# Kernel tuning notes

Measured on AMD Instinct MI355X. Metric: run time of the kernel, lower is better.

The kernel has to match this reference:

```python
import jax, jax.numpy as jnp
import numpy as np

NUM_TOKENS = 32000
DIM = 1024
DEPTH = 4
HEADS = 16
DIM_HEAD = 64
FF_MULT = 4
DH_FF = int(DIM * FF_MULT * 2 / 3)  # 2730
B, N = 2, 2048
ROPE_THETA = 10000.0


def setup_inputs() -> dict:
    key = jax.random.key(0)
    ks = jax.random.split(key, 8)
    s = 0.02
    return {
        "tokens": jax.random.randint(ks[0], (B, N), 0, NUM_TOKENS),
        "token_emb": jax.random.normal(ks[1], (NUM_TOKENS, DIM)) * s,
        "attn_norm_w": jnp.ones((DEPTH, DIM)),
        "wqkv": jax.random.normal(ks[2], (DEPTH, DIM, 3 * HEADS * DIM_HEAD)) * s,
        "wo": jax.random.normal(ks[3], (DEPTH, HEADS * DIM_HEAD, DIM)) * s,
        "ff_norm_w": jnp.ones((DEPTH, DIM)),
        "ff_w1": jax.random.normal(ks[4], (DEPTH, DIM, 2 * DH_FF)) * s,
        "ff_b1": jnp.zeros((DEPTH, 2 * DH_FF)),
        "ff_w2": jax.random.normal(ks[5], (DEPTH, DH_FF, DIM)) * s,
        "ff_b2": jnp.zeros((DEPTH, DIM)),
        "final_norm_w": jnp.ones((DIM,)),
        "logits_w": jax.random.normal(ks[6], (DIM, NUM_TOKENS)) * s,
        "logits_b": jnp.zeros((NUM_TOKENS,)),
    }


def rmsnorm(x, w):
    eps = jnp.finfo(x.dtype).eps  # torch RMSNorm default eps
    var = jnp.mean(jnp.square(x), axis=-1, keepdims=True)
    return x * jax.lax.rsqrt(var + eps) * w


def rotate_half(x):
    x1, x2 = jnp.split(x, 2, axis=-1)
    return jnp.concatenate((-x2, x1), axis=-1)


def apply_rope(pos, t):
    return t * jnp.cos(pos) + rotate_half(t) * jnp.sin(pos)


def reference(tokens, token_emb, attn_norm_w, wqkv, wo, ff_norm_w,
              ff_w1, ff_b1, ff_w2, ff_b2, final_norm_w, logits_w, logits_b):
    b, n = tokens.shape
    x = token_emb[tokens]  # [b, n, dim]

    # rotary embedding table [n, dim_head]
    inv_freq = ROPE_THETA ** (-(jnp.arange(0, DIM_HEAD, 2, dtype=jnp.float32) / DIM_HEAD))
    freqs = jnp.arange(n, dtype=jnp.float32)[:, None] * inv_freq[None, :]
    pos = jnp.concatenate((freqs, freqs), axis=-1)

    scale = DIM_HEAD ** -0.5
    causal = jnp.triu(jnp.ones((n, n), dtype=bool), 1)

    for l in range(DEPTH):
        # --- attention ---
        h = rmsnorm(x, attn_norm_w[l])
        qkv = jnp.einsum('bnd,de->bne', h, wqkv[l])
        qkv = qkv.reshape(b, n, 3, HEADS, DIM_HEAD)
        qkv = jnp.transpose(qkv, (2, 0, 3, 1, 4))  # [3, b, h, n, d]
        q, k, v = qkv[0], qkv[1], qkv[2]
        q = apply_rope(pos, q)
        k = apply_rope(pos, k)
        q = q * scale
        sim = jnp.einsum('bhid,bhjd->bhij', q, k)
        sim = jnp.where(causal, -jnp.finfo(sim.dtype).max, sim)
        attn = jax.nn.softmax(sim, axis=-1)
        out = jnp.einsum('bhij,bhjd->bhid', attn, v)
        out = jnp.transpose(out, (0, 2, 1, 3)).reshape(b, n, HEADS * DIM_HEAD)
        x = jnp.einsum('bne,ed->bnd', out, wo[l]) + x

        # --- GEGLU feedforward ---
        h = rmsnorm(x, ff_norm_w[l])
        u = jnp.einsum('bnd,de->bne', h, ff_w1[l]) + ff_b1[l]
        u1, gate = jnp.split(u, 2, axis=-1)
        g = jax.nn.gelu(gate, approximate=False) * u1
        x = jnp.einsum('bne,ed->bnd', g, ff_w2[l]) + ff_b2[l] + x

    embed = rmsnorm(x, final_norm_w)
    logits = jnp.einsum('bnd,dv->bnv', embed, logits_w) + logits_b
    return logits
```

## Files before the change

kernel.cpp:

```cpp
#include <hip/hip_runtime.h>
#include <math.h>
#include <stdint.h>


using short8v = __attribute__((ext_vector_type(8))) short;
using f32x4   = __attribute__((ext_vector_type(4))) float;

__device__ __forceinline__ float b2f(short s) {
    union { unsigned u; float f; } v; v.u = ((unsigned)(unsigned short)s) << 16; return v.f;
}
__device__ __forceinline__ short f2b(float f) {
    union { float f; unsigned u; } v; v.f = f;
    unsigned r = v.u + 0x7FFFu + ((v.u >> 16) & 1u);
    return (short)(r >> 16);
}

__device__ __forceinline__ void mfma_n(f32x4& d, short8v a, short8v b) {
    asm("v_mfma_f32_16x16x32_bf16 %0, %1, %2, %0" : "+v"(d) : "v"(a), "v"(b));
}
__device__ __forceinline__ void mfma_f(f32x4& d, short8v a, short8v b) {
    asm("s_nop 1\n\tv_mfma_f32_16x16x32_bf16 %0, %1, %2, %0" : "+v"(d) : "v"(a), "v"(b));
}
#define MFMA_FENCE() do { __builtin_amdgcn_sched_barrier(0); \
    asm volatile("s_nop 7\n\ts_nop 7"); \
    __builtin_amdgcn_sched_barrier(0); } while (0)

__device__ __forceinline__ void gload16(const void* g, void* l) {
    __builtin_amdgcn_global_load_lds(
        (const __attribute__((address_space(1))) unsigned int*)(uintptr_t)g,
        (__attribute__((address_space(3))) unsigned int*)(uintptr_t)l,
        16, 0, 0);
}

__global__ void rope_table_k(float* __restrict__ ct, float* __restrict__ st) {
    int i = blockIdx.x * 256 + threadIdx.x;
    int n = i >> 5, j = i & 31;
    float freq = expf(-(float)j * (9.210340371976184f / 32.f));
    float a = (float)n * freq;
    ct[i] = cosf(a);
    st[i] = sinf(a);
}

__global__ void embed_k(const int* __restrict__ tok, const float* __restrict__ emb,
                        float* __restrict__ x) {
    int row = blockIdx.x;
    int tk = tok[row];
    const float4* src = (const float4*)(emb + (size_t)tk * 1024);
    float4* dst = (float4*)(x + (size_t)row * 1024);
    dst[threadIdx.x] = src[threadIdx.x];
}

__global__ void wconv_k(const float* __restrict__ W, short* __restrict__ T,
                        int K, int N, int Kpad,
                        size_t w_lstride, size_t t_lstride) {
    W += blockIdx.z * w_lstride;
    T += blockIdx.z * t_lstride;
    int n0 = blockIdx.x * 32, k0 = blockIdx.y * 32;
    __shared__ float tile[32][33];
    int t = threadIdx.x;
    int kk = t >> 3, ns = (t & 7) * 4;
    float4 v = make_float4(0.f, 0.f, 0.f, 0.f);
    int gk = k0 + kk;
    if (gk < K) {
        if (n0 + ns + 3 < N) {
            v = *(const float4*)(W + (size_t)gk * N + n0 + ns);
        } else {
            float tmp[4] = {0.f, 0.f, 0.f, 0.f};
            #pragma unroll
            for (int j = 0; j < 4; ++j)
                if (n0 + ns + j < N) tmp[j] = W[(size_t)gk * N + n0 + ns + j];
            v = make_float4(tmp[0], tmp[1], tmp[2], tmp[3]);
        }
    }
    tile[kk][ns + 0] = v.x; tile[kk][ns + 1] = v.y;
    tile[kk][ns + 2] = v.z; tile[kk][ns + 3] = v.w;
    __syncthreads();
    int nn = t >> 3, ks = (t & 7) * 4;
    short o[4];
    #pragma unroll
    for (int j = 0; j < 4; ++j) o[j] = f2b(tile[ks + j][nn]);
    *(int2*)(T + (size_t)(n0 + nn) * Kpad + k0 + ks) = *(int2*)o;
}

__global__ void rmsnorm_k(const float* __restrict__ x, const float* __restrict__ wt,
                          short* __restrict__ out) {
    int row = blockIdx.x;
    int t = threadIdx.x;
    const float* xr = x + (size_t)row * 1024;
    float4 v = ((const float4*)xr)[t];
    float ss = v.x * v.x + v.y * v.y + v.z * v.z + v.w * v.w;
    #pragma unroll
    for (int off = 32; off > 0; off >>= 1) ss += __shfl_down(ss, off, 64);
    __shared__ float red[4];
    if ((t & 63) == 0) red[t >> 6] = ss;
    __syncthreads();
    float tot = red[0] + red[1] + red[2] + red[3];
    float inv = rsqrtf(tot * (1.f / 1024.f) + 1.1920929e-7f);
    float4 wv = ((const float4*)wt)[t];
    int2 pk;
    pk.x = (int)(unsigned short)f2b(v.x * inv * wv.x) |
           ((int)(unsigned short)f2b(v.y * inv * wv.y) << 16);
    pk.y = (int)(unsigned short)f2b(v.z * inv * wv.z) |
           ((int)(unsigned short)f2b(v.w * inv * wv.w) << 16);
    *(int2*)(out + (size_t)row * 1024 + t * 4) = pk;
}

__global__ void rope_apply_k(short* __restrict__ qkv, const float* __restrict__ ct,
                             const float* __restrict__ st) {
    int gidx = blockIdx.x * 256 + threadIdx.x;
    int j  = gidx & 31;
    int r  = (gidx >> 5) & 4095;
    int hk = gidx >> 17;
    int qk = hk >> 4, h = hk & 15;
    int n = r & 2047;
    size_t base = (size_t)r * 3072 + (size_t)qk * 1024 + h * 64 + j;
    float a  = b2f(qkv[base]);
    float bv = b2f(qkv[base + 32]);
    float cc = ct[n * 32 + j], sv = st[n * 32 + j];
    float na = a * cc - bv * sv;
    float nb = bv * cc + a * sv;
    if (qk == 0) { na *= 0.125f; nb *= 0.125f; }
    qkv[base]      = f2b(na);
    qkv[base + 32] = f2b(nb);
}

__global__ void vt_k(const short* __restrict__ qkv, short* __restrict__ vt) {
    int id = blockIdx.x * 256 + threadIdx.x;
    int dt = id & 7, nt = (id >> 3) & 255, bh = id >> 11;
    int b = bh >> 4, h = bh & 15;
    short s[8][8];
    #pragma unroll
    for (int r = 0; r < 8; ++r)
        *(int4*)s[r] = *(const int4*)(qkv + (size_t)(b * 2048 + nt * 8 + r) * 3072
                                      + 2048 + h * 64 + dt * 8);
    #pragma unroll
    for (int cc = 0; cc < 8; ++cc) {
        short o4[8];
        #pragma unroll
        for (int r = 0; r < 8; ++r) o4[r] = s[r][cc];
        *(int4*)(vt + (size_t)(bh * 64 + dt * 8 + cc) * 2048 + nt * 8) = *(int4*)o4;
    }
}

__global__ void geglu_k(const short* __restrict__ u, short* __restrict__ gbuf) {
    int r = blockIdx.x;
    int c = blockIdx.y * 256 + threadIdx.x;
    if (c >= 2752) return;
    float v = 0.f;
    if (c < 2730) {
        float u1 = b2f(u[(size_t)r * 5460 + c]);
        float gt = b2f(u[(size_t)r * 5460 + 2730 + c]);
        v = 0.5f * gt * (1.f + erff(gt * 0.7071067811865475f)) * u1;
    }
    gbuf[(size_t)r * 2752 + c] = f2b(v);
}

template <bool BIAS, bool RES, bool OUTBF16>
__global__ __launch_bounds__(256, 2) void gemm2(
    const short* __restrict__ A, const short* __restrict__ Bt,
    const float* __restrict__ bias, const float* __restrict__ res,
    void* __restrict__ outp, int N, int lda, int ldb, int ksteps) {
    __shared__ __align__(16) short As[128 * 32];
    __shared__ __align__(16) short Bs[128 * 32];
    const int t = threadIdx.x;
    const int lane = t & 63;
    const int w = t >> 6, wm = w >> 1, wn = w & 1;
    const int c = lane & 15, g = lane >> 4;

    const int nwg = (int)gridDim.x;
    const int cpx = nwg >> 3;
    const int wg = ((int)blockIdx.x & 7) * cpx + ((int)blockIdx.x >> 3);
    const int m0 = (wg & 31) << 7;
    const int n0 = (wg >> 5) << 7;

    const int srow = w * 32 + (lane >> 2);
    const int sseg = (lane & 3) * 8;
    const short* ga0 = A  + (size_t)(m0 + srow) * lda + sseg;
    const short* ga1 = A  + (size_t)(m0 + srow + 16) * lda + sseg;
    const short* gb0 = Bt + (size_t)(n0 + srow) * ldb + sseg;
    const short* gb1 = Bt + (size_t)(n0 + srow + 16) * ldb + sseg;
    short* la0 = &As[(w * 2 + 0) * 512];
    short* la1 = &As[(w * 2 + 1) * 512];
    short* lb0 = &Bs[(w * 2 + 0) * 512];
    short* lb1 = &Bs[(w * 2 + 1) * 512];

    f32x4 acc[4][4] = {};

    for (int kt = 0; kt < ksteps; ++kt) {
        const int k0 = kt << 5;
        __syncthreads();
        gload16(ga0 + k0, la0);
        gload16(ga1 + k0, la1);
        gload16(gb0 + k0, lb0);
        gload16(gb1 + k0, lb1);
        __syncthreads();
        short8v af[4], bf[4];
        #pragma unroll
        for (int mi = 0; mi < 4; ++mi)
            af[mi] = *(const short8v*)&As[(wm * 64 + mi * 16 + c) * 32 + g * 8];
        #pragma unroll
        for (int ni = 0; ni < 4; ++ni)
            bf[ni] = *(const short8v*)&Bs[(wn * 64 + ni * 16 + c) * 32 + g * 8];
        #pragma unroll
        for (int mi = 0; mi < 4; ++mi)
            #pragma unroll
            for (int ni = 0; ni < 4; ++ni)
                mfma_n(acc[mi][ni], af[mi], bf[ni]);
    }
    MFMA_FENCE();
    #pragma unroll
    for (int mi = 0; mi < 4; ++mi) {
        #pragma unroll
        for (int ni = 0; ni < 4; ++ni) {
            int col = n0 + wn * 64 + ni * 16 + c;
            if (col < N) {
                float bv = BIAS ? bias[col] : 0.f;
                #pragma unroll
                for (int i = 0; i < 4; ++i) {
                    int row = m0 + wm * 64 + mi * 16 + g * 4 + i;
                    size_t off = (size_t)row * N + col;
                    float v = acc[mi][ni][i] + bv;
                    if (RES) v += res[off];
                    if (OUTBF16) ((short*)outp)[off] = f2b(v);
                    else         ((float*)outp)[off] = v;
                }
            }
        }
    }
}

__global__ __launch_bounds__(256, 2) void attn_fwd(
    const short* __restrict__ qkv, const short* __restrict__ vt,
    short* __restrict__ o) {
    const int qt = blockIdx.x, bh = blockIdx.y;
    const int b = bh >> 4, h = bh & 15;
    const int t = threadIdx.x, lane = t & 63, w = t >> 6;
    const int c = lane & 15, g = lane >> 4;
    __shared__ __align__(16) short Ks[128 * 72];
    __shared__ __align__(16) short Vs[64 * 136];
    __shared__ __align__(16) short Ps[128 * 136];

    #pragma unroll
    for (int i = 0; i < 4; ++i) {
        int idx = t + i * 256, r = idx >> 3, seg = idx & 7;
        *(int4*)&Ps[r * 136 + seg * 8] =
            *(const int4*)(qkv + (size_t)(b * 2048 + qt * 128 + r) * 3072 + h * 64 + seg * 8);
    }
    __syncthreads();
    short8v qf[2][2];
    #pragma unroll
    for (int mi = 0; mi < 2; ++mi)
        #pragma unroll
        for (int kk = 0; kk < 2; ++kk)
            qf[mi][kk] = *(const short8v*)&Ps[(w * 32 + mi * 16 + c) * 136 + kk * 32 + g * 8];

    f32x4 oacc[2][4] = {};
    float mrow[2][4], lrow[2][4];
    #pragma unroll
    for (int mi = 0; mi < 2; ++mi)
        #pragma unroll
        for (int i = 0; i < 4; ++i) { mrow[mi][i] = -3.0e38f; lrow[mi][i] = 0.f; }

    for (int jt = 0; jt <= qt; ++jt) {
        __syncthreads();
        #pragma unroll
        for (int i = 0; i < 4; ++i) {
            int idx = t + i * 256, r = idx >> 3, seg = idx & 7;
            *(int4*)&Ks[r * 72 + seg * 8] =
                *(const int4*)(qkv + (size_t)(b * 2048 + jt * 128 + r) * 3072
                               + 1024 + h * 64 + seg * 8);
        }
        #pragma unroll
        for (int i = 0; i < 4; ++i) {
            int idx = t + i * 256, d = idx >> 4, seg = idx & 15;
            *(int4*)&Vs[d * 136 + seg * 8] =
                *(const int4*)(vt + (size_t)(bh * 64 + d) * 2048 + jt * 128 + seg * 8);
        }
        __syncthreads();
        f32x4 sacc[2][8] = {};
        #pragma unroll
        for (int kk = 0; kk < 2; ++kk) {
            short8v kf[8];
            #pragma unroll
            for (int ni = 0; ni < 8; ++ni)
                kf[ni] = *(const short8v*)&Ks[(ni * 16 + c) * 72 + kk * 32 + g * 8];
            #pragma unroll
            for (int mi = 0; mi < 2; ++mi)
                #pragma unroll
                for (int ni = 0; ni < 8; ++ni) {
                    if (kk == 0) mfma_f(sacc[mi][ni], qf[mi][kk], kf[ni]);
                    else         mfma_n(sacc[mi][ni], qf[mi][kk], kf[ni]);
                }
        }
        MFMA_FENCE();
        if (jt == qt) {
            #pragma unroll
            for (int mi = 0; mi < 2; ++mi)
                #pragma unroll
                for (int ni = 0; ni < 8; ++ni)
                    #pragma unroll
                    for (int i = 0; i < 4; ++i) {
                        int qrow = w * 32 + mi * 16 + g * 4 + i;
                        int kcol = ni * 16 + c;
                        if (kcol > qrow) sacc[mi][ni][i] = -3.0e38f;
                    }
        }
        #pragma unroll
        for (int mi = 0; mi < 2; ++mi) {
            #pragma unroll
            for (int i = 0; i < 4; ++i) {
                float mx = sacc[mi][0][i];
                #pragma unroll
                for (int ni = 1; ni < 8; ++ni) mx = fmaxf(mx, sacc[mi][ni][i]);
                #pragma unroll
                for (int off = 1; off < 16; off <<= 1) mx = fmaxf(mx, __shfl_xor(mx, off, 64));
                float mnew = fmaxf(mrow[mi][i], mx);
                float alpha = __expf(mrow[mi][i] - mnew);
                mrow[mi][i] = mnew;
                float ls = 0.f;
                #pragma unroll
                for (int ni = 0; ni < 8; ++ni) {
                    float p = __expf(sacc[mi][ni][i] - mnew);
                    sacc[mi][ni][i] = p;
                    ls += p;
                }
                #pragma unroll
                for (int off = 1; off < 16; off <<= 1) ls += __shfl_xor(ls, off, 64);
                lrow[mi][i] = lrow[mi][i] * alpha + ls;
                #pragma unroll
                for (int df = 0; df < 4; ++df) oacc[mi][df][i] *= alpha;
            }
        }
        #pragma unroll
        for (int mi = 0; mi < 2; ++mi)
            #pragma unroll
            for (int ni = 0; ni < 8; ++ni)
                #pragma unroll
                for (int i = 0; i < 4; ++i)
                    Ps[(w * 32 + mi * 16 + g * 4 + i) * 136 + ni * 16 + c] =
                        f2b(sacc[mi][ni][i]);
        #pragma unroll
        for (int kk = 0; kk < 4; ++kk) {
            short8v pf[2], vf[4];
            #pragma unroll
            for (int mi = 0; mi < 2; ++mi)
                pf[mi] = *(const short8v*)&Ps[(w * 32 + mi * 16 + c) * 136 + kk * 32 + g * 8];
            #pragma unroll
            for (int df = 0; df < 4; ++df)
                vf[df] = *(const short8v*)&Vs[(df * 16 + c) * 136 + kk * 32 + g * 8];
            #pragma unroll
            for (int mi = 0; mi < 2; ++mi)
                #pragma unroll
                for (int df = 0; df < 4; ++df) {
                    if (kk == 0) mfma_f(oacc[mi][df], pf[mi], vf[df]);
                    else         mfma_n(oacc[mi][df], pf[mi], vf[df]);
                }
        }
    }
    MFMA_FENCE();
    #pragma unroll
    for (int mi = 0; mi < 2; ++mi)
        #pragma unroll
        for (int df = 0; df < 4; ++df)
            #pragma unroll
            for (int i = 0; i < 4; ++i) {
                int qrow = qt * 128 + w * 32 + mi * 16 + g * 4 + i;
                float v = oacc[mi][df][i] / lrow[mi][i];
                o[(size_t)(b * 2048 + qrow) * 1024 + h * 64 + df * 16 + c] = f2b(v);
            }
}

extern "C" void kernel_launch(void* const* d_in, const int* in_sizes, int n_in,
                              void* d_out, int out_size, void* d_ws, size_t ws_size,
                              hipStream_t stream) {
    (void)in_sizes; (void)n_in; (void)out_size; (void)ws_size;
    const int*   tokens = (const int*)d_in[0];
    const float* temb   = (const float*)d_in[1];
    const float* anw    = (const float*)d_in[2];
    const float* wqkv   = (const float*)d_in[3];
    const float* wo     = (const float*)d_in[4];
    const float* fnw    = (const float*)d_in[5];
    const float* fw1    = (const float*)d_in[6];
    const float* fb1    = (const float*)d_in[7];
    const float* fw2    = (const float*)d_in[8];
    const float* fb2    = (const float*)d_in[9];
    const float* finw   = (const float*)d_in[10];
    const float* lw     = (const float*)d_in[11];
    const float* lb     = (const float*)d_in[12];

    char* ws = (char*)d_ws;
    float* x    = (float*)(ws + 0);
    short* hb   = (short*)(ws + 16777216);
    short* qkv  = (short*)(ws + 25165824);
    short* ao   = (short*)(ws + 50331648);
    short* ub   = (short*)(ws + 58720256);
    short* gb   = (short*)(ws + 103448576);
    short* vtb  = (short*)(ws + 125992960);
    float* ct   = (float*)(ws + 134381568);
    float* st   = (float*)(ws + 134643712);
    short* qkvT = (short*)(ws + 134905856);
    short* woT  = (short*)(ws + 160071680);
    short* fw1T = (short*)(ws + 168460288);
    short* fw2T = (short*)(ws + 213549056);
    short* logT = (short*)(ws + 236093440);

    rope_table_k<<<256, 256, 0, stream>>>(ct, st);
    embed_k<<<4096, 256, 0, stream>>>(tokens, temb, x);

    wconv_k<<<dim3(96, 32, 4), 256, 0, stream>>>(
        wqkv, qkvT, 1024, 3072, 1024, (size_t)1024 * 3072, (size_t)3072 * 1024);
    wconv_k<<<dim3(32, 32, 4), 256, 0, stream>>>(
        wo, woT, 1024, 1024, 1024, (size_t)1024 * 1024, (size_t)1024 * 1024);
    wconv_k<<<dim3(172, 32, 4), 256, 0, stream>>>(
        fw1, fw1T, 1024, 5460, 1024, (size_t)1024 * 5460, (size_t)5504 * 1024);
    wconv_k<<<dim3(32, 86, 4), 256, 0, stream>>>(
        fw2, fw2T, 2730, 1024, 2752, (size_t)2730 * 1024, (size_t)1024 * 2752);
    wconv_k<<<dim3(1000, 32, 1), 256, 0, stream>>>(
        lw, logT, 1024, 32000, 1024, 0, 0);

    for (int l = 0; l < 4; ++l) {
        rmsnorm_k<<<4096, 256, 0, stream>>>(x, anw + l * 1024, hb);
        gemm2<false, false, true><<<32 * 24, 256, 0, stream>>>(
            hb, qkvT + (size_t)l * 3072 * 1024, nullptr, nullptr, qkv, 3072, 1024, 1024, 32);
        rope_apply_k<<<16384, 256, 0, stream>>>(qkv, ct, st);
        vt_k<<<256, 256, 0, stream>>>(qkv, vtb);
        attn_fwd<<<dim3(16, 32), 256, 0, stream>>>(qkv, vtb, ao);
        gemm2<false, true, false><<<32 * 8, 256, 0, stream>>>(
            ao, woT + (size_t)l * 1024 * 1024, nullptr, x, x, 1024, 1024, 1024, 32);
        rmsnorm_k<<<4096, 256, 0, stream>>>(x, fnw + l * 1024, hb);
        gemm2<true, false, true><<<32 * 43, 256, 0, stream>>>(
            hb, fw1T + (size_t)l * 5504 * 1024, fb1 + l * 5460, nullptr, ub, 5460, 1024, 1024, 32);
        geglu_k<<<dim3(4096, 11), 256, 0, stream>>>(ub, gb);
        gemm2<true, true, false><<<32 * 8, 256, 0, stream>>>(
            gb, fw2T + (size_t)l * 1024 * 2752, fb2 + l * 1024, x, x, 1024, 2752, 2752, 86);
    }
    rmsnorm_k<<<4096, 256, 0, stream>>>(x, finw, hb);
    gemm2<true, false, false><<<32 * 250, 256, 0, stream>>>(
        hb, logT, lb, nullptr, d_out, 32000, 1024, 1024, 32);
}
```

Baseline: 2.105 ms.

## Add 256x128-tile 8-wave GEMM with interleaved LDS prefetch for wide GEMMs

```diff
diff --git a/kernel.cpp b/kernel.cpp
--- a/kernel.cpp
+++ b/kernel.cpp
@@ -31,6 +31,12 @@
         (__attribute__((address_space(3))) unsigned int*)(uintptr_t)l,
         16, 0, 0);
 }
+
+#define BARX() do { asm volatile("" ::: "memory"); \
+    __builtin_amdgcn_s_barrier(); asm volatile("" ::: "memory"); } while (0)
+#define VMN(n) asm volatile("s_waitcnt vmcnt(" #n ")" ::: "memory")
+#define LGKM0() do { asm volatile("s_waitcnt lgkmcnt(0)" ::: "memory"); \
+    __builtin_amdgcn_sched_barrier(0); } while (0)
 
 __global__ void rope_table_k(float* __restrict__ ct, float* __restrict__ st) {
     int i = blockIdx.x * 256 + threadIdx.x;
@@ -229,6 +235,184 @@
     }
 }
 
+template <bool BIAS, bool RES, bool OUTBF16>
+__global__ __launch_bounds__(512, 1) void gemm3(
+    const short* __restrict__ A, const short* __restrict__ Bt,
+    const float* __restrict__ bias, const float* __restrict__ res,
+    void* __restrict__ outp, int N, int lda, int ldb, int nrowsB, int KT) {
+    __shared__ __align__(16) short L[49152];
+    const int t = threadIdx.x;
+    const int lane = t & 63;
+    const int w = t >> 6;
+    const int wm = w >> 2, wn = w & 3;
+    const int c = lane & 15, g = lane >> 4;
+
+    const int nwg = (int)gridDim.x, cpx = nwg >> 3;
+    const int wg = ((int)blockIdx.x & 7) * cpx + ((int)blockIdx.x >> 3);
+    const int m0 = (wg & 31) << 7;
+    const int n0 = (wg >> 5) << 8;
+
+    const int rS = t >> 3, sS = t & 7;
+    const int sSw = (sS ^ (rS & 7)) << 3;
+    size_t aoffh[2], broff[2][2];
+    #pragma unroll
+    for (int h = 0; h < 2; ++h)
+        aoffh[h] = (size_t)(m0 + h * 64 + rS) * lda + sSw;
+    #pragma unroll
+    for (int h = 0; h < 2; ++h)
+        #pragma unroll
+        for (int i = 0; i < 2; ++i) {
+            int brow = n0 + h * 128 + rS + i * 64;
+            if (brow > nrowsB - 1) brow = nrowsB - 1;
+            broff[h][i] = (size_t)brow * ldb + sSw;
+        }
+    short* ldsA[2][2];
+    short* ldsB[2][2];
+    #pragma unroll
+    for (int p = 0; p < 2; ++p)
+        #pragma unroll
+        for (int h = 0; h < 2; ++h) {
+            ldsA[p][h] = &L[(p * 2 + h) * 4096 + w * 512];
+            ldsB[p][h] = &L[16384 + (p * 2 + h) * 8192 + w * 512];
+        }
+
+    const int cb0 = ((g * 8) ^ ((c & 7) * 8));
+    const int vbA0 = wm * 4096 + c * 64 + cb0;
+    const int vbA1 = vbA0 ^ 32;
+    const int vbB0 = 16384 + (wn >> 1) * 8192 + (wn & 1) * 4096 + c * 64 + cb0;
+    const int vbB1 = vbB0 ^ 32;
+
+    #define STA3(p, h, kt) gload16(A + aoffh[h] + (kt) * 64, ldsA[p][h])
+    #define STB3(p, h, kt) do { \
+        gload16(Bt + broff[h][0] + (kt) * 64, ldsB[p][h]); \
+        gload16(Bt + broff[h][1] + (kt) * 64, ldsB[p][h] + 4096); } while (0)
+    #define LDA3(p, mi, ks) (*(const short8v*)&L[(p) * 8192 + (mi) * 1024 + ((ks) ? vbA1 : vbA0)])
+    #define LDB3(p, ni, ks) (*(const short8v*)&L[(p) * 16384 + (ni) * 1024 + ((ks) ? vbB1 : vbB0)])
+    #define MFMA8(MLO, NLO, BV) do { \
+        _Pragma("unroll") for (int ks_ = 0; ks_ < 2; ++ks_) \
+        _Pragma("unroll") for (int mi_ = 0; mi_ < 2; ++mi_) \
+        _Pragma("unroll") for (int ni_ = 0; ni_ < 2; ++ni_) \
+            mfma_n(acc[(MLO) + mi_][(NLO) + ni_], av[(MLO) + mi_][ks_], BV[(NLO) + ni_][ks_]); \
+        } while (0)
+
+    f32x4 acc[4][4] = {};
+    short8v av[4][2], bc[4][2], bn[4][2];
+
+    STB3(0, 1, 0); STB3(0, 0, 0); STA3(0, 0, 0); STA3(0, 1, 0);
+    STB3(1, 1, 1); STB3(1, 0, 1); STA3(1, 0, 1); STA3(1, 1, 1);
+    VMN(6);
+    BARX();
+    #pragma unroll
+    for (int ni = 0; ni < 4; ++ni)
+        #pragma unroll
+        for (int ks = 0; ks < 2; ++ks)
+            bc[ni][ks] = LDB3(0, ni, ks);
+    LGKM0();
+    BARX();
+    asm volatile("s_nop 7\n\ts_nop 7");
+
+    for (int KB = 0; KB < KT; KB += 2) {
+        const bool st1 = (KB + 2 < KT);
+        const bool st2 = (KB + 3 < KT);
+        #pragma unroll
+        for (int mi = 0; mi < 2; ++mi)
+            #pragma unroll
+            for (int ks = 0; ks < 2; ++ks) av[mi][ks] = LDA3(0, mi, ks);
+        if (st1) STB3(0, 1, KB + 2);
+        BARX();
+        __builtin_amdgcn_s_setprio(1); MFMA8(0, 0, bc); __builtin_amdgcn_s_setprio(0);
+        BARX();
+        #pragma unroll
+        for (int mi = 2; mi < 4; ++mi)
+            #pragma unroll
+            for (int ks = 0; ks < 2; ++ks) av[mi][ks] = LDA3(0, mi, ks);
+        if (st1) { STB3(0, 0, KB + 2); VMN(6); } else { VMN(2); }
+        BARX();
+        __builtin_amdgcn_s_setprio(1); MFMA8(2, 0, bc); __builtin_amdgcn_s_setprio(0);
+        BARX();
+        #pragma unroll
+        for (int ni = 0; ni < 2; ++ni)
+            #pragma unroll
+            for (int ks = 0; ks < 2; ++ks) bn[ni][ks] = LDB3(1, ni, ks);
+        if (st1) STA3(0, 0, KB + 2);
+        BARX();
+        __builtin_amdgcn_s_setprio(1); MFMA8(0, 2, bc); __builtin_amdgcn_s_setprio(0);
+        BARX();
+        #pragma unroll
+        for (int ni = 2; ni < 4; ++ni)
+            #pragma unroll
+            for (int ks = 0; ks < 2; ++ks) bn[ni][ks] = LDB3(1, ni, ks);
+        if (st1) { STA3(0, 1, KB + 2); VMN(6); } else { VMN(0); }
+        BARX();
+        __builtin_amdgcn_s_setprio(1); MFMA8(2, 2, bc); __builtin_amdgcn_s_setprio(0);
+        BARX();
+        #pragma unroll
+        for (int mi = 0; mi < 2; ++mi)
+            #pragma unroll
+            for (int ks = 0; ks < 2; ++ks) av[mi][ks] = LDA3(1, mi, ks);
+        if (st2) STB3(1, 1, KB + 3);
+        BARX();
+        __builtin_amdgcn_s_setprio(1); MFMA8(0, 0, bn); __builtin_amdgcn_s_setprio(0);
+        BARX();
+        #pragma unroll
+        for (int mi = 2; mi < 4; ++mi)
+            #pragma unroll
+            for (int ks = 0; ks < 2; ++ks) av[mi][ks] = LDA3(1, mi, ks);
+        if (st2) STB3(1, 0, KB + 3);
+        if (st1) VMN(6);
+        BARX();
+        __builtin_amdgcn_s_setprio(1); MFMA8(2, 0, bn); __builtin_amdgcn_s_setprio(0);
+        BARX();
+        if (st1) {
+            #pragma unroll
+            for (int ni = 0; ni < 2; ++ni)
+                #pragma unroll
+                for (int ks = 0; ks < 2; ++ks) bc[ni][ks] = LDB3(0, ni, ks);
+        }
+        if (st2) STA3(1, 0, KB + 3);
+        BARX();
+        __builtin_amdgcn_s_setprio(1); MFMA8(0, 2, bn); __builtin_amdgcn_s_setprio(0);
+        BARX();
+        if (st1) {
+            #pragma unroll
+            for (int ni = 2; ni < 4; ++ni)
+                #pragma unroll
+                for (int ks = 0; ks < 2; ++ks) bc[ni][ks] = LDB3(0, ni, ks);
+        }
+        if (st2) STA3(1, 1, KB + 3);
+        if (st1) VMN(6);
+        BARX();
+        __builtin_amdgcn_s_setprio(1); MFMA8(2, 2, bn); __builtin_amdgcn_s_setprio(0);
+        BARX();
+    }
+
+    MFMA_FENCE();
+    #pragma unroll
+    for (int mi = 0; mi < 4; ++mi) {
+        #pragma unroll
+        for (int ni = 0; ni < 4; ++ni) {
+            int col = n0 + wn * 64 + ni * 16 + c;
+            if (col < N) {
+                float bv = BIAS ? bias[col] : 0.f;
+                #pragma unroll
+                for (int i = 0; i < 4; ++i) {
+                    int row = m0 + wm * 64 + mi * 16 + g * 4 + i;
+                    size_t off = (size_t)row * N + col;
+                    float v = acc[mi][ni][i] + bv;
+                    if (RES) v += res[off];
+                    if (OUTBF16) ((short*)outp)[off] = f2b(v);
+                    else         ((float*)outp)[off] = v;
+                }
+            }
+        }
+    }
+    #undef STA3
+    #undef STB3
+    #undef LDA3
+    #undef LDB3
+    #undef MFMA8
+}
+
 __global__ __launch_bounds__(256, 2) void attn_fwd(
     const short* __restrict__ qkv, const short* __restrict__ vt,
     short* __restrict__ o) {
@@ -420,21 +604,23 @@
 
     for (int l = 0; l < 4; ++l) {
         rmsnorm_k<<<4096, 256, 0, stream>>>(x, anw + l * 1024, hb);
-        gemm2<false, false, true><<<32 * 24, 256, 0, stream>>>(
-            hb, qkvT + (size_t)l * 3072 * 1024, nullptr, nullptr, qkv, 3072, 1024, 1024, 32);
+        gemm3<false, false, true><<<32 * 12, 512, 0, stream>>>(
+            hb, qkvT + (size_t)l * 3072 * 1024, nullptr, nullptr, qkv,
+            3072, 1024, 1024, 3072, 16);
         rope_apply_k<<<16384, 256, 0, stream>>>(qkv, ct, st);
         vt_k<<<256, 256, 0, stream>>>(qkv, vtb);
         attn_fwd<<<dim3(16, 32), 256, 0, stream>>>(qkv, vtb, ao);
         gemm2<false, true, false><<<32 * 8, 256, 0, stream>>>(
             ao, woT + (size_t)l * 1024 * 1024, nullptr, x, x, 1024, 1024, 1024, 32);
         rmsnorm_k<<<4096, 256, 0, stream>>>(x, fnw + l * 1024, hb);
-        gemm2<true, false, true><<<32 * 43, 256, 0, stream>>>(
-            hb, fw1T + (size_t)l * 5504 * 1024, fb1 + l * 5460, nullptr, ub, 5460, 1024, 1024, 32);
+        gemm3<true, false, true><<<32 * 22, 512, 0, stream>>>(
+            hb, fw1T + (size_t)l * 5504 * 1024, fb1 + l * 5460, nullptr, ub,
+            5460, 1024, 1024, 5504, 16);
         geglu_k<<<dim3(4096, 11), 256, 0, stream>>>(ub, gb);
         gemm2<true, true, false><<<32 * 8, 256, 0, stream>>>(
             gb, fw2T + (size_t)l * 1024 * 2752, fb2 + l * 1024, x, x, 1024, 2752, 2752, 86);
     }
     rmsnorm_k<<<4096, 256, 0, stream>>>(x, finw, hb);
-    gemm2<true, false, false><<<32 * 250, 256, 0, stream>>>(
-        hb, logT, lb, nullptr, d_out, 32000, 1024, 1024, 32);
-}
+    gemm3<true, false, false><<<32 * 125, 512, 0, stream>>>(
+        hb, logT, lb, nullptr, d_out, 32000, 1024, 1024, 32000, 16);
+}
```

After: 2.059 ms. -2.2%, faster.

## Add 256x256-tile 8-wave GEMM with double-buffered LDS for QKV, FF1 and logits

Applied to the files above, without the earlier changes.

```diff
diff --git a/kernel.cpp b/kernel.cpp
--- a/kernel.cpp
+++ b/kernel.cpp
@@ -31,6 +31,10 @@
         (__attribute__((address_space(3))) unsigned int*)(uintptr_t)l,
         16, 0, 0);
 }
+
+#define BARX() do { asm volatile("" ::: "memory"); \
+    __builtin_amdgcn_s_barrier(); asm volatile("" ::: "memory"); } while (0)
+#define VMN(n) asm volatile("s_waitcnt vmcnt(" #n ")" ::: "memory")
 
 __global__ void rope_table_k(float* __restrict__ ct, float* __restrict__ st) {
     int i = blockIdx.x * 256 + threadIdx.x;
@@ -229,6 +233,119 @@
     }
 }
 
+template <bool BIAS, bool RES, bool OUTBF16>
+__global__ __launch_bounds__(512, 2) void gemm4(
+    const short* __restrict__ A, const short* __restrict__ Bt,
+    const float* __restrict__ bias, const float* __restrict__ res,
+    void* __restrict__ outp, int N, int lda, int ldb, int nrowsB, int KT) {
+    __shared__ __align__(16) short L[65536];
+    const int t = threadIdx.x;
+    const int lane = t & 63;
+    const int w = t >> 6;
+    const int wm = w >> 2, wn = w & 3;
+    const int c = lane & 15, g = lane >> 4;
+
+    const int nwg = (int)gridDim.x, cpx = nwg >> 3;
+    const int wg = ((int)blockIdx.x & 7) * cpx + ((int)blockIdx.x >> 3);
+    const int m0 = (wg & 15) << 8;
+    const int n0 = (wg >> 4) << 8;
+
+    const int sub0 = t & 63;
+    const int seg0 = sub0 >> 4, r0 = sub0 & 15;
+    const int slab0 = t >> 6, slab1 = slab0 + 8;
+    const size_t aoff0 = (size_t)(m0 + slab0 * 16 + r0) * lda + seg0 * 8;
+    const size_t aoff1 = (size_t)(m0 + slab1 * 16 + r0) * lda + seg0 * 8;
+    int br0 = n0 + slab0 * 16 + r0; if (br0 > nrowsB - 1) br0 = nrowsB - 1;
+    int br1 = n0 + slab1 * 16 + r0; if (br1 > nrowsB - 1) br1 = nrowsB - 1;
+    const size_t boff0 = (size_t)br0 * ldb + seg0 * 8;
+    const size_t boff1 = (size_t)br1 * ldb + seg0 * 8;
+
+    char* Lb = (char*)L;
+    const int rb = g * 256 + c * 16;
+
+    #define STA4(p, kh, kt) do { \
+        gload16(A + aoff0 + (kt) * 64 + (kh) * 32, Lb + ((p)*2+(kh))*16384 + w*1024); \
+        gload16(A + aoff1 + (kt) * 64 + (kh) * 32, Lb + ((p)*2+(kh))*16384 + 8192 + w*1024); } while (0)
+    #define STB4(p, kh, kt) do { \
+        gload16(Bt + boff0 + (kt) * 64 + (kh) * 32, Lb + 65536 + ((p)*2+(kh))*16384 + w*1024); \
+        gload16(Bt + boff1 + (kt) * 64 + (kh) * 32, Lb + 65536 + ((p)*2+(kh))*16384 + 8192 + w*1024); } while (0)
+    #define LDA4(p, ks, mi) (*(const short8v*)(Lb + ((p)*2+(ks))*16384 + (wm*8+(mi))*1024 + rb))
+    #define LDB4(p, ks, ni) (*(const short8v*)(Lb + 65536 + ((p)*2+(ks))*16384 + (wn*4+(ni))*1024 + rb))
+    #define MFMAQ(MB) do { \
+        _Pragma("unroll") for (int mi_ = 0; mi_ < 4; ++mi_) \
+        _Pragma("unroll") for (int ni_ = 0; ni_ < 4; ++ni_) \
+            mfma_n(acc[(MB) + mi_][ni_], av[mi_], bv[ni_]); } while (0)
+
+    f32x4 acc[8][4] = {};
+    short8v av[4], bv[4];
+
+    STA4(0, 0, 0); STB4(0, 0, 0); STA4(0, 1, 0); STB4(0, 1, 0);
+    VMN(4);
+    BARX();
+    asm volatile("s_nop 7\n\ts_nop 7");
+
+    #define TILE4(p, pn, tc, stg2) do { \
+         \
+        _Pragma("unroll") for (int mi = 0; mi < 4; ++mi) av[mi] = LDA4(p, 0, mi); \
+        _Pragma("unroll") for (int ni = 0; ni < 4; ++ni) bv[ni] = LDB4(p, 0, ni); \
+        if (stg2) STA4(pn, 0, (tc) + 1); \
+        BARX(); \
+        __builtin_amdgcn_s_setprio(1); MFMAQ(0); __builtin_amdgcn_s_setprio(0); \
+        BARX(); \
+         \
+        _Pragma("unroll") for (int mi = 0; mi < 4; ++mi) av[mi] = LDA4(p, 0, mi + 4); \
+        if (stg2) { STB4(pn, 0, (tc) + 1); VMN(4); } else { VMN(0); } \
+        BARX(); \
+        __builtin_amdgcn_s_setprio(1); MFMAQ(4); __builtin_amdgcn_s_setprio(0); \
+        BARX(); \
+         \
+        _Pragma("unroll") for (int mi = 0; mi < 4; ++mi) av[mi] = LDA4(p, 1, mi); \
+        _Pragma("unroll") for (int ni = 0; ni < 4; ++ni) bv[ni] = LDB4(p, 1, ni); \
+        if (stg2) STA4(pn, 1, (tc) + 1); \
+        BARX(); \
+        __builtin_amdgcn_s_setprio(1); MFMAQ(0); __builtin_amdgcn_s_setprio(0); \
+        BARX(); \
+         \
+        _Pragma("unroll") for (int mi = 0; mi < 4; ++mi) av[mi] = LDA4(p, 1, mi + 4); \
+        if (stg2) { STB4(pn, 1, (tc) + 1); VMN(4); } \
+        BARX(); \
+        __builtin_amdgcn_s_setprio(1); MFMAQ(4); __builtin_amdgcn_s_setprio(0); \
+        BARX(); \
+    } while (0)
+
+    for (int kt = 0; kt < KT; kt += 2) {
+        TILE4(0, 1, kt, true);
+        TILE4(1, 0, kt + 1, (kt + 2 < KT));
+    }
+    #undef TILE4
+
+    MFMA_FENCE();
+    #pragma unroll
+    for (int mi = 0; mi < 8; ++mi) {
+        #pragma unroll
+        for (int ni = 0; ni < 4; ++ni) {
+            int col = n0 + wn * 64 + ni * 16 + c;
+            if (col < N) {
+                float bvv = BIAS ? bias[col] : 0.f;
+                #pragma unroll
+                for (int i = 0; i < 4; ++i) {
+                    int row = m0 + wm * 128 + mi * 16 + g * 4 + i;
+                    size_t off = (size_t)row * N + col;
+                    float v = acc[mi][ni][i] + bvv;
+                    if (RES) v += res[off];
+                    if (OUTBF16) ((short*)outp)[off] = f2b(v);
+                    else         ((float*)outp)[off] = v;
+                }
+            }
+        }
+    }
+    #undef STA4
+    #undef STB4
+    #undef LDA4
+    #undef LDB4
+    #undef MFMAQ
+}
+
 __global__ __launch_bounds__(256, 2) void attn_fwd(
     const short* __restrict__ qkv, const short* __restrict__ vt,
     short* __restrict__ o) {
@@ -401,8 +518,8 @@
     short* qkvT = (short*)(ws + 134905856);
     short* woT  = (short*)(ws + 160071680);
     short* fw1T = (short*)(ws + 168460288);
-    short* fw2T = (short*)(ws + 213549056);
-    short* logT = (short*)(ws + 236093440);
+    short* fw2T = (short*)(ws + 214597632);
+    short* logT = (short*)(ws + 237142016);
 
     rope_table_k<<<256, 256, 0, stream>>>(ct, st);
     embed_k<<<4096, 256, 0, stream>>>(tokens, temb, x);
@@ -411,8 +528,8 @@
         wqkv, qkvT, 1024, 3072, 1024, (size_t)1024 * 3072, (size_t)3072 * 1024);
     wconv_k<<<dim3(32, 32, 4), 256, 0, stream>>>(
         wo, woT, 1024, 1024, 1024, (size_t)1024 * 1024, (size_t)1024 * 1024);
-    wconv_k<<<dim3(172, 32, 4), 256, 0, stream>>>(
-        fw1, fw1T, 1024, 5460, 1024, (size_t)1024 * 5460, (size_t)5504 * 1024);
+    wconv_k<<<dim3(176, 32, 4), 256, 0, stream>>>(
+        fw1, fw1T, 1024, 5460, 1024, (size_t)1024 * 5460, (size_t)5632 * 1024);
     wconv_k<<<dim3(32, 86, 4), 256, 0, stream>>>(
         fw2, fw2T, 2730, 1024, 2752, (size_t)2730 * 1024, (size_t)1024 * 2752);
     wconv_k<<<dim3(1000, 32, 1), 256, 0, stream>>>(
@@ -420,21 +537,23 @@
 
     for (int l = 0; l < 4; ++l) {
         rmsnorm_k<<<4096, 256, 0, stream>>>(x, anw + l * 1024, hb);
-        gemm2<false, false, true><<<32 * 24, 256, 0, stream>>>(
-            hb, qkvT + (size_t)l * 3072 * 1024, nullptr, nullptr, qkv, 3072, 1024, 1024, 32);
+        gemm4<false, false, true><<<192, 512, 0, stream>>>(
+            hb, qkvT + (size_t)l * 3072 * 1024, nullptr, nullptr, qkv,
+            3072, 1024, 1024, 3072, 16);
         rope_apply_k<<<16384, 256, 0, stream>>>(qkv, ct, st);
         vt_k<<<256, 256, 0, stream>>>(qkv, vtb);
         attn_fwd<<<dim3(16, 32), 256, 0, stream>>>(qkv, vtb, ao);
         gemm2<false, true, false><<<32 * 8, 256, 0, stream>>>(
             ao, woT + (size_t)l * 1024 * 1024, nullptr, x, x, 1024, 1024, 1024, 32);
         rmsnorm_k<<<4096, 256, 0, stream>>>(x, fnw + l * 1024, hb);
-        gemm2<true, false, true><<<32 * 43, 256, 0, stream>>>(
-            hb, fw1T + (size_t)l * 5504 * 1024, fb1 + l * 5460, nullptr, ub, 5460, 1024, 1024, 32);
+        gemm4<true, false, true><<<352, 512, 0, stream>>>(
+            hb, fw1T + (size_t)l * 5632 * 1024, fb1 + l * 5460, nullptr, ub,
+            5460, 1024, 1024, 5632, 16);
         geglu_k<<<dim3(4096, 11), 256, 0, stream>>>(ub, gb);
         gemm2<true, true, false><<<32 * 8, 256, 0, stream>>>(
             gb, fw2T + (size_t)l * 1024 * 2752, fb2 + l * 1024, x, x, 1024, 2752, 2752, 86);
     }
     rmsnorm_k<<<4096, 256, 0, stream>>>(x, finw, hb);
-    gemm2<true, false, false><<<32 * 250, 256, 0, stream>>>(
-        hb, logT, lb, nullptr, d_out, 32000, 1024, 1024, 32);
-}
+    gemm4<true, false, false><<<2000, 512, 0, stream>>>(
+        hb, logT, lb, nullptr, d_out, 32000, 1024, 1024, 32000, 16);
+}
```

After: 2.112 ms. About the same (+0.3%).

## Double GEMM K-tile to 64 and fuse RoPE into QKV GEMM epilogue

Applied to the files above, without the earlier changes.

```diff
diff --git a/kernel.cpp b/kernel.cpp
--- a/kernel.cpp
+++ b/kernel.cpp
@@ -105,25 +105,6 @@
     *(int2*)(out + (size_t)row * 1024 + t * 4) = pk;
 }
 
-__global__ void rope_apply_k(short* __restrict__ qkv, const float* __restrict__ ct,
-                             const float* __restrict__ st) {
-    int gidx = blockIdx.x * 256 + threadIdx.x;
-    int j  = gidx & 31;
-    int r  = (gidx >> 5) & 4095;
-    int hk = gidx >> 17;
-    int qk = hk >> 4, h = hk & 15;
-    int n = r & 2047;
-    size_t base = (size_t)r * 3072 + (size_t)qk * 1024 + h * 64 + j;
-    float a  = b2f(qkv[base]);
-    float bv = b2f(qkv[base + 32]);
-    float cc = ct[n * 32 + j], sv = st[n * 32 + j];
-    float na = a * cc - bv * sv;
-    float nb = bv * cc + a * sv;
-    if (qk == 0) { na *= 0.125f; nb *= 0.125f; }
-    qkv[base]      = f2b(na);
-    qkv[base + 32] = f2b(nb);
-}
-
 __global__ void vt_k(const short* __restrict__ qkv, short* __restrict__ vt) {
     int id = blockIdx.x * 256 + threadIdx.x;
     int dt = id & 7, nt = (id >> 3) & 255, bh = id >> 11;
@@ -155,71 +136,114 @@
     gbuf[(size_t)r * 2752 + c] = f2b(v);
 }
 
-template <bool BIAS, bool RES, bool OUTBF16>
-__global__ __launch_bounds__(256, 2) void gemm2(
+template <bool BIAS, bool RES, bool OUTBF16, bool ROPE>
+__global__ __launch_bounds__(256, 2) void gemm5(
     const short* __restrict__ A, const short* __restrict__ Bt,
     const float* __restrict__ bias, const float* __restrict__ res,
-    void* __restrict__ outp, int N, int lda, int ldb, int ksteps) {
-    __shared__ __align__(16) short As[128 * 32];
-    __shared__ __align__(16) short Bs[128 * 32];
+    void* __restrict__ outp, int N, int lda, int ldb, int ksteps,
+    const float* __restrict__ ct, const float* __restrict__ st) {
+    __shared__ __align__(16) short L5[16384];
     const int t = threadIdx.x;
     const int lane = t & 63;
     const int w = t >> 6, wm = w >> 1, wn = w & 1;
     const int c = lane & 15, g = lane >> 4;
 
-    const int nwg = (int)gridDim.x;
-    const int cpx = nwg >> 3;
+    const int nwg = (int)gridDim.x, cpx = nwg >> 3;
     const int wg = ((int)blockIdx.x & 7) * cpx + ((int)blockIdx.x >> 3);
     const int m0 = (wg & 31) << 7;
     const int n0 = (wg >> 5) << 7;
 
-    const int srow = w * 32 + (lane >> 2);
-    const int sseg = (lane & 3) * 8;
-    const short* ga0 = A  + (size_t)(m0 + srow) * lda + sseg;
-    const short* ga1 = A  + (size_t)(m0 + srow + 16) * lda + sseg;
-    const short* gb0 = Bt + (size_t)(n0 + srow) * ldb + sseg;
-    const short* gb1 = Bt + (size_t)(n0 + srow + 16) * ldb + sseg;
-    short* la0 = &As[(w * 2 + 0) * 512];
-    short* la1 = &As[(w * 2 + 1) * 512];
-    short* lb0 = &Bs[(w * 2 + 0) * 512];
-    short* lb1 = &Bs[(w * 2 + 1) * 512];
+    const int sr = lane & 15, sg = lane >> 4;
+    size_t aG[4], bG[4];
+    char *aL[4], *bL[4];
+    #pragma unroll
+    for (int j = 0; j < 4; ++j) {
+        int q = w * 4 + j;
+        int slab = q & 7, kh = q >> 3;
+        aG[j] = (size_t)(m0 + slab * 16 + sr) * lda + kh * 32 + sg * 8;
+        bG[j] = (size_t)(n0 + slab * 16 + sr) * ldb + kh * 32 + sg * 8;
+        aL[j] = (char*)L5 + q * 1024;
+        bL[j] = (char*)L5 + 16384 + q * 1024;
+    }
+    const int rb = g * 256 + c * 16;
 
     f32x4 acc[4][4] = {};
+    short8v av[4], bv[4];
 
     for (int kt = 0; kt < ksteps; ++kt) {
-        const int k0 = kt << 5;
+        const int k0 = kt << 6;
         __syncthreads();
-        gload16(ga0 + k0, la0);
-        gload16(ga1 + k0, la1);
-        gload16(gb0 + k0, lb0);
-        gload16(gb1 + k0, lb1);
+        #pragma unroll
+        for (int j = 0; j < 4; ++j) gload16(A + aG[j] + k0, aL[j]);
+        #pragma unroll
+        for (int j = 0; j < 4; ++j) gload16(Bt + bG[j] + k0, bL[j]);
         __syncthreads();
-        short8v af[4], bf[4];
-        #pragma unroll
-        for (int mi = 0; mi < 4; ++mi)
-            af[mi] = *(const short8v*)&As[(wm * 64 + mi * 16 + c) * 32 + g * 8];
-        #pragma unroll
-        for (int ni = 0; ni < 4; ++ni)
-            bf[ni] = *(const short8v*)&Bs[(wn * 64 + ni * 16 + c) * 32 + g * 8];
-        #pragma unroll
-        for (int mi = 0; mi < 4; ++mi)
+        #pragma unroll
+        for (int kh = 0; kh < 2; ++kh) {
+            #pragma unroll
+            for (int mi = 0; mi < 4; ++mi)
+                av[mi] = *(const short8v*)((char*)L5 + kh * 8192 + (wm * 4 + mi) * 1024 + rb);
             #pragma unroll
             for (int ni = 0; ni < 4; ++ni)
-                mfma_n(acc[mi][ni], af[mi], bf[ni]);
+                bv[ni] = *(const short8v*)((char*)L5 + 16384 + kh * 8192 + (wn * 4 + ni) * 1024 + rb);
+            #pragma unroll
+            for (int mi = 0; mi < 4; ++mi)
+                #pragma unroll
+                for (int ni = 0; ni < 4; ++ni)
+                    mfma_n(acc[mi][ni], av[mi], bv[ni]);
+        }
     }
     MFMA_FENCE();
+
+    if (ROPE) {
+        const int colbase = n0 + wn * 64;
+        const int sec = colbase >> 10;
+        if (sec < 2) {
+            const float sc = (sec == 0) ? 0.125f : 1.0f;
+            #pragma unroll
+            for (int mi = 0; mi < 4; ++mi)
+                #pragma unroll
+                for (int ni = 0; ni < 2; ++ni) {
+                    const int col = colbase + ni * 16 + c;
+                    const int jj = ni * 16 + c;
+                    #pragma unroll
+                    for (int i = 0; i < 4; ++i) {
+                        int row = m0 + wm * 64 + mi * 16 + g * 4 + i;
+                        int n = row & 2047;
+                        float cv = ct[n * 32 + jj], sv = st[n * 32 + jj];
+                        float a = acc[mi][ni][i], b = acc[mi][ni + 2][i];
+                        ((short*)outp)[(size_t)row * N + col]      = f2b((a * cv - b * sv) * sc);
+                        ((short*)outp)[(size_t)row * N + col + 32] = f2b((b * cv + a * sv) * sc);
+                    }
+                }
+        } else {
+            #pragma unroll
+            for (int mi = 0; mi < 4; ++mi)
+                #pragma unroll
+                for (int ni = 0; ni < 4; ++ni) {
+                    int col = colbase + ni * 16 + c;
+                    #pragma unroll
+                    for (int i = 0; i < 4; ++i) {
+                        int row = m0 + wm * 64 + mi * 16 + g * 4 + i;
+                        ((short*)outp)[(size_t)row * N + col] = f2b(acc[mi][ni][i]);
+                    }
+                }
+        }
+        return;
+    }
+
     #pragma unroll
     for (int mi = 0; mi < 4; ++mi) {
         #pragma unroll
         for (int ni = 0; ni < 4; ++ni) {
             int col = n0 + wn * 64 + ni * 16 + c;
             if (col < N) {
-                float bv = BIAS ? bias[col] : 0.f;
+                float bvv = BIAS ? bias[col] : 0.f;
                 #pragma unroll
                 for (int i = 0; i < 4; ++i) {
                     int row = m0 + wm * 64 + mi * 16 + g * 4 + i;
                     size_t off = (size_t)row * N + col;
-                    float v = acc[mi][ni][i] + bv;
+                    float v = acc[mi][ni][i] + bvv;
                     if (RES) v += res[off];
                     if (OUTBF16) ((short*)outp)[off] = f2b(v);
                     else         ((float*)outp)[off] = v;
@@ -401,8 +425,8 @@
     short* qkvT = (short*)(ws + 134905856);
     short* woT  = (short*)(ws + 160071680);
     short* fw1T = (short*)(ws + 168460288);
-    short* fw2T = (short*)(ws + 213549056);
-    short* logT = (short*)(ws + 236093440);
+    short* fw2T = (short*)(ws + 214597632);
+    short* logT = (short*)(ws + 237142016);
 
     rope_table_k<<<256, 256, 0, stream>>>(ct, st);
     embed_k<<<4096, 256, 0, stream>>>(tokens, temb, x);
@@ -411,8 +435,8 @@
         wqkv, qkvT, 1024, 3072, 1024, (size_t)1024 * 3072, (size_t)3072 * 1024);
     wconv_k<<<dim3(32, 32, 4), 256, 0, stream>>>(
         wo, woT, 1024, 1024, 1024, (size_t)1024 * 1024, (size_t)1024 * 1024);
-    wconv_k<<<dim3(172, 32, 4), 256, 0, stream>>>(
-        fw1, fw1T, 1024, 5460, 1024, (size_t)1024 * 5460, (size_t)5504 * 1024);
+    wconv_k<<<dim3(176, 32, 4), 256, 0, stream>>>(
+        fw1, fw1T, 1024, 5460, 1024, (size_t)1024 * 5460, (size_t)5632 * 1024);
     wconv_k<<<dim3(32, 86, 4), 256, 0, stream>>>(
         fw2, fw2T, 2730, 1024, 2752, (size_t)2730 * 1024, (size_t)1024 * 2752);
     wconv_k<<<dim3(1000, 32, 1), 256, 0, stream>>>(
@@ -420,21 +444,24 @@
 
     for (int l = 0; l < 4; ++l) {
         rmsnorm_k<<<4096, 256, 0, stream>>>(x, anw + l * 1024, hb);
-        gemm2<false, false, true><<<32 * 24, 256, 0, stream>>>(
-            hb, qkvT + (size_t)l * 3072 * 1024, nullptr, nullptr, qkv, 3072, 1024, 1024, 32);
-        rope_apply_k<<<16384, 256, 0, stream>>>(qkv, ct, st);
+        gemm5<false, false, true, true><<<32 * 24, 256, 0, stream>>>(
+            hb, qkvT + (size_t)l * 3072 * 1024, nullptr, nullptr, qkv,
+            3072, 1024, 1024, 16, ct, st);
         vt_k<<<256, 256, 0, stream>>>(qkv, vtb);
         attn_fwd<<<dim3(16, 32), 256, 0, stream>>>(qkv, vtb, ao);
-        gemm2<false, true, false><<<32 * 8, 256, 0, stream>>>(
-            ao, woT + (size_t)l * 1024 * 1024, nullptr, x, x, 1024, 1024, 1024, 32);
+        gemm5<false, true, false, false><<<32 * 8, 256, 0, stream>>>(
+            ao, woT + (size_t)l * 1024 * 1024, nullptr, x, x,
+            1024, 1024, 1024, 16, nullptr, nullptr);
         rmsnorm_k<<<4096, 256, 0, stream>>>(x, fnw + l * 1024, hb);
-        gemm2<true, false, true><<<32 * 43, 256, 0, stream>>>(
-            hb, fw1T + (size_t)l * 5504 * 1024, fb1 + l * 5460, nullptr, ub, 5460, 1024, 1024, 32);
+        gemm5<true, false, true, false><<<32 * 43, 256, 0, stream>>>(
+            hb, fw1T + (size_t)l * 5632 * 1024, fb1 + l * 5460, nullptr, ub,
+            5460, 1024, 1024, 16, nullptr, nullptr);
         geglu_k<<<dim3(4096, 11), 256, 0, stream>>>(ub, gb);
-        gemm2<true, true, false><<<32 * 8, 256, 0, stream>>>(
-            gb, fw2T + (size_t)l * 1024 * 2752, fb2 + l * 1024, x, x, 1024, 2752, 2752, 86);
+        gemm5<true, true, false, false><<<32 * 8, 256, 0, stream>>>(
+            gb, fw2T + (size_t)l * 1024 * 2752, fb2 + l * 1024, x, x,
+            1024, 2752, 2752, 43, nullptr, nullptr);
     }
     rmsnorm_k<<<4096, 256, 0, stream>>>(x, finw, hb);
-    gemm2<true, false, false><<<32 * 250, 256, 0, stream>>>(
-        hb, logT, lb, nullptr, d_out, 32000, 1024, 1024, 32);
-}
+    gemm5<true, false, false, false><<<32 * 250, 256, 0, stream>>>(
+        hb, logT, lb, nullptr, d_out, 32000, 1024, 1024, 16, nullptr, nullptr);
+}
```

New measurement: 2.332 ms. 1.11x slower.
